# Performance work log

Hardware: AMD Instinct MI355X
Metric: run time of the kernel (lower is better)

## Reference

```python
import jax, jax.numpy as jnp
import numpy as np
import math

D_MODEL = 1024
N_HEADS = 16
SLOT_DIM = 64
N_SLOTS = 1024
TOP_K = 2
LN_EPS = 1e-5


def setup_inputs() -> dict:
    key = jax.random.key(0)
    ks = jax.random.split(key, 8)
    x = jax.random.normal(ks[0], (4, 2048, D_MODEL), dtype=jnp.float32)
    ln_gamma = jnp.ones((D_MODEL,), jnp.float32)
    ln_beta = jnp.zeros((D_MODEL,), jnp.float32)
    q_w = jax.random.normal(ks[1], (N_HEADS * SLOT_DIM, D_MODEL), jnp.float32) / math.sqrt(D_MODEL)
    q_b = jnp.zeros((N_HEADS * SLOT_DIM,), jnp.float32)
    slot_signatures = jax.random.normal(ks[2], (N_HEADS, N_SLOTS, SLOT_DIM), jnp.float32) * 0.5
    slot_values = jax.random.normal(ks[3], (N_HEADS, N_SLOTS, SLOT_DIM), jnp.float32) * 0.02
    out_w = jax.random.normal(ks[4], (D_MODEL, N_HEADS * SLOT_DIM), jnp.float32) / math.sqrt(N_HEADS * SLOT_DIM)
    out_b = jnp.zeros((D_MODEL,), jnp.float32)
    temperature = jnp.ones((1,), jnp.float32)
    return {"x": x, "ln_gamma": ln_gamma, "ln_beta": ln_beta, "q_w": q_w, "q_b": q_b,
            "slot_signatures": slot_signatures, "slot_values": slot_values,
            "out_w": out_w, "out_b": out_b, "temperature": temperature}


def _ternary_ste(sig):
    # forward = {-1,0,+1} quantization; backward = identity (straight-through)
    q = jnp.where(sig > 0.3, 1.0, jnp.where(sig < -0.3, -1.0, 0.0))
    return sig + jax.lax.stop_gradient(q - sig)


def reference(x, ln_gamma, ln_beta, q_w, q_b, slot_signatures, slot_values, out_w, out_b, temperature):
    B, T, D = x.shape
    # LayerNorm
    mean = jnp.mean(x, axis=-1, keepdims=True)
    var = jnp.var(x, axis=-1, keepdims=True)
    x_norm = (x - mean) * jax.lax.rsqrt(var + LN_EPS) * ln_gamma + ln_beta
    # Query projection -> [B, T, H, slot_dim]
    q = (x_norm @ q_w.T + q_b).reshape(B, T, N_HEADS, SLOT_DIM)
    sigs = _ternary_ste(slot_signatures)  # [H, S, d]
    scores = jnp.einsum('bthd,hsd->bths', q, sigs)
    scores = scores / (temperature * math.sqrt(SLOT_DIM))  # [B, T, H, S]
    # top-k routing
    topk_scores, slot_idx = jax.lax.top_k(scores, TOP_K)  # [B, T, H, K]
    weights = jax.nn.softmax(topk_scores, axis=-1)
    # gather selected slot values: [B, T, H, K, d]
    h_idx = jnp.arange(N_HEADS)[None, None, :, None]
    selected = slot_values[h_idx, slot_idx]
    read = jnp.sum(selected * weights[..., None], axis=3)  # [B, T, H, d]
    read = read.reshape(B, T, N_HEADS * SLOT_DIM)
    out = read @ out_w.T + out_b
    return x + out
```

## Files before the change

kernel.cpp:

```cpp
#include <hip/hip_runtime.h>

typedef unsigned short u16;
typedef unsigned int   u32;
typedef float f32x4 __attribute__((ext_vector_type(4)));
typedef __bf16 bf16x8 __attribute__((ext_vector_type(8)));

__device__ __forceinline__ u16 f2bf(float f){
  u32 u = __float_as_uint(f);
  u += 0x7fffu + ((u >> 16) & 1u);
  return (u16)(u >> 16);
}

__device__ __forceinline__ void gld16(const void* g, void* l){
  __builtin_amdgcn_global_load_lds((const __attribute__((address_space(1))) u32*)g,
                                   (__attribute__((address_space(3))) u32*)l, 16, 0, 0);
}

__global__ __launch_bounds__(256) void convert_kernel(
    const float* __restrict__ qw, const float* __restrict__ ow,
    const float* __restrict__ sg,
    u16* __restrict__ qwb, u16* __restrict__ owb, u16* __restrict__ sgb){
  int i = blockIdx.x * 256 + threadIdx.x;
  qwb[i] = f2bf(qw[i]);
  owb[i] = f2bf(ow[i]);
  float s = sg[i];
  float t = (s > 0.3f) ? 1.0f : ((s < -0.3f) ? -1.0f : 0.0f);
  sgb[i] = f2bf(t);
}

__global__ __launch_bounds__(256) void ln_kernel(
    const float* __restrict__ x, const float* __restrict__ g,
    const float* __restrict__ b, u16* __restrict__ xn){
  const int t = blockIdx.x, tid = threadIdx.x;
  f32x4 v = *(const f32x4*)(x + (size_t)t * 1024 + tid * 4);
  float s  = v[0] + v[1] + v[2] + v[3];
  float ss = v[0]*v[0] + v[1]*v[1] + v[2]*v[2] + v[3]*v[3];
  for (int off = 32; off; off >>= 1){
    s  += __shfl_down(s, off);
    ss += __shfl_down(ss, off);
  }
  __shared__ float red[8];
  int w = tid >> 6;
  if ((tid & 63) == 0){ red[w] = s; red[4 + w] = ss; }
  __syncthreads();
  s  = red[0] + red[1] + red[2] + red[3];
  ss = red[4] + red[5] + red[6] + red[7];
  float mean = s * (1.0f / 1024.0f);
  float var  = ss * (1.0f / 1024.0f) - mean * mean;
  float rs   = rsqrtf(var + 1e-5f);
  f32x4 gv = *(const f32x4*)(g + tid * 4);
  f32x4 bv = *(const f32x4*)(b + tid * 4);
  float y0 = (v[0]-mean)*rs*gv[0]+bv[0];
  float y1 = (v[1]-mean)*rs*gv[1]+bv[1];
  float y2 = (v[2]-mean)*rs*gv[2]+bv[2];
  float y3 = (v[3]-mean)*rs*gv[3]+bv[3];
  uint2 pk;
  pk.x = (u32)f2bf(y0) | ((u32)f2bf(y1) << 16);
  pk.y = (u32)f2bf(y2) | ((u32)f2bf(y3) << 16);
  *(uint2*)(xn + (size_t)t * 1024 + tid * 4) = pk;
}

__global__ __launch_bounds__(256, 2) void gemm_bt(
    const u16* __restrict__ A, const u16* __restrict__ B,
    const float* __restrict__ bias, const float* __restrict__ resid,
    float* __restrict__ outf, u16* __restrict__ outb, int mode){
  __shared__ u16 As[128 * 64];
  __shared__ u16 Bs[128 * 64];
  const int tid = threadIdx.x;
  const int m0 = blockIdx.y * 128, n0 = blockIdx.x * 128;
  const int w = tid >> 6, lane = tid & 63, lm = lane & 15, quad = lane >> 4;
  const int wm = (w & 1) * 64, wn = (w >> 1) * 64;
  const int lr = lane >> 3;
  const int lg = (lane & 7) ^ lr;
  const f32x4 fz = {0.f, 0.f, 0.f, 0.f};
  f32x4 acc[4][4];
  #pragma unroll
  for (int i = 0; i < 4; ++i)
    #pragma unroll
    for (int j = 0; j < 4; ++j) acc[i][j] = fz;

  const u16* gA = A + (size_t)(m0 + w * 32 + lr) * 1024 + lg * 8;
  const u16* gB = B + (size_t)(n0 + w * 32 + lr) * 1024 + lg * 8;
  u16* lA = &As[(w * 32) * 64];
  u16* lB = &Bs[(w * 32) * 64];
  const int sw = lm & 7;

  for (int kt = 0; kt < 16; ++kt){
    #pragma unroll
    for (int sub = 0; sub < 4; ++sub){
      gld16(gA + (size_t)(sub * 8) * 1024 + kt * 64, lA + sub * 8 * 64);
      gld16(gB + (size_t)(sub * 8) * 1024 + kt * 64, lB + sub * 8 * 64);
    }
    __syncthreads();
    #pragma unroll
    for (int kk = 0; kk < 2; ++kk){
      const int ch = ((quad + kk * 4) ^ sw) * 8;
      bf16x8 afr[4], bfr[4];
      #pragma unroll
      for (int i = 0; i < 4; ++i)
        afr[i] = *(const bf16x8*)(&As[(wm + i * 16 + lm) * 64 + ch]);
      #pragma unroll
      for (int j = 0; j < 4; ++j)
        bfr[j] = *(const bf16x8*)(&Bs[(wn + j * 16 + lm) * 64 + ch]);
      #pragma unroll
      for (int i = 0; i < 4; ++i)
        #pragma unroll
        for (int j = 0; j < 4; ++j)
          acc[i][j] = __builtin_amdgcn_mfma_f32_16x16x32_bf16(afr[i], bfr[j], acc[i][j], 0, 0, 0);
    }
    __syncthreads();
  }

  #pragma unroll
  for (int i = 0; i < 4; ++i){
    #pragma unroll
    for (int r = 0; r < 4; ++r){
      int grow = m0 + wm + i * 16 + quad * 4 + r;
      #pragma unroll
      for (int j = 0; j < 4; ++j){
        int gcol = n0 + wn + j * 16 + lm;
        float v = acc[i][j][r] + bias[gcol];
        if (mode){
          v += resid[(size_t)grow * 1024 + gcol];
          outf[(size_t)grow * 1024 + gcol] = v;
        } else {
          outb[(size_t)grow * 1024 + gcol] = f2bf(v);
        }
      }
    }
  }
}

__global__ __launch_bounds__(256) void route_kernel(
    const u16* __restrict__ q, const u16* __restrict__ sig,
    const float* __restrict__ V, const float* __restrict__ temp,
    u16* __restrict__ rd){
  const int h = blockIdx.y;
  const int t0 = blockIdx.x * 64;
  const int tid = threadIdx.x, w = tid >> 6, lane = tid & 63;
  const int lm = lane & 15, quad = lane >> 4;

  __shared__ u16 sbuf[2][64 * 64];
  __shared__ float fw1[64], fw2[64];
  __shared__ int   fi1[64], fi2[64];

  const u16* qrow = q + (size_t)(t0 + w * 16 + lm) * 1024 + h * 64;
  bf16x8 a0 = *(const bf16x8*)(qrow + quad * 8);
  bf16x8 a1 = *(const bf16x8*)(qrow + 32 + quad * 8);

  const u16* sigh = sig + (size_t)h * 65536;

  auto stage = [&](int t, int b){
    #pragma unroll
    for (int r = 0; r < 2; ++r){
      int c = tid + r * 256;
      int s = c >> 3, gl = c & 7;
      int g = gl ^ (s & 7);
      uint4 v = *(const uint4*)(sigh + (size_t)t * 4096 + s * 64 + g * 8);
      *(uint4*)(&sbuf[b][c * 8]) = v;
    }
  };

  float v1[4], v2[4]; int j1[4], j2[4];
  #pragma unroll
  for (int r = 0; r < 4; ++r){ v1[r] = -3e38f; v2[r] = -3e38f; j1[r] = 0; j2[r] = 0; }

  const int swz = lm & 7;
  stage(0, 0);
  for (int t = 0; t < 16; ++t){
    __syncthreads();
    if (t + 1 < 16) stage(t + 1, (t + 1) & 1);
    const u16* buf = sbuf[t & 1];
    #pragma unroll
    for (int ss = 0; ss < 4; ++ss){
      int srow = ss * 16 + lm;
      int c0 = (quad ^ swz) * 8;
      bf16x8 b0 = *(const bf16x8*)(&buf[srow * 64 + c0]);
      bf16x8 b1 = *(const bf16x8*)(&buf[srow * 64 + (c0 ^ 32)]);
      f32x4 acc = {0.f, 0.f, 0.f, 0.f};
      acc = __builtin_amdgcn_mfma_f32_16x16x32_bf16(a0, b0, acc, 0, 0, 0);
      acc = __builtin_amdgcn_mfma_f32_16x16x32_bf16(a1, b1, acc, 0, 0, 0);
      int sidx = t * 64 + srow;
      #pragma unroll
      for (int r = 0; r < 4; ++r){
        float v = acc[r];
        bool g1 = v > v1[r];
        bool g2 = v > v2[r];
        float nv2 = g1 ? v1[r] : (g2 ? v : v2[r]);
        int   nj2 = g1 ? j1[r] : (g2 ? sidx : j2[r]);
        v2[r] = nv2; j2[r] = nj2;
        v1[r] = g1 ? v : v1[r];
        j1[r] = g1 ? sidx : j1[r];
      }
    }
  }
  #pragma unroll
  for (int off = 1; off < 16; off <<= 1){
    #pragma unroll
    for (int r = 0; r < 4; ++r){
      float ov1 = __shfl_xor(v1[r], off);
      int   oj1 = __shfl_xor(j1[r], off);
      float ov2 = __shfl_xor(v2[r], off);
      int   oj2 = __shfl_xor(j2[r], off);
      bool gt = ov1 > v1[r];
      float ca = gt ? v1[r] : ov1; int cja = gt ? j1[r] : oj1;
      float cb = gt ? ov2  : v2[r]; int cjb = gt ? oj2  : j2[r];
      v1[r] = gt ? ov1 : v1[r];  j1[r] = gt ? oj1 : j1[r];
      bool gb = cb > ca;
      v2[r] = gb ? cb : ca;  j2[r] = gb ? cjb : cja;
    }
  }
  if (lm == 0){
    float tsc = 1.0f / (temp[0] * 8.0f);
    #pragma unroll
    for (int r = 0; r < 4; ++r){
      int tok = w * 16 + quad * 4 + r;
      float ex = expf((v2[r] - v1[r]) * tsc);
      float iw = 1.0f / (1.0f + ex);
      fw1[tok] = iw; fw2[tok] = ex * iw;
      fi1[tok] = j1[r]; fi2[tok] = j2[r];
    }
  }
  __syncthreads();
  int tok = tid >> 2, d0 = (tid & 3) * 16;
  const float* va = V + ((size_t)h * 1024 + fi1[tok]) * 64 + d0;
  const float* vb = V + ((size_t)h * 1024 + fi2[tok]) * 64 + d0;
  float W1 = fw1[tok], W2 = fw2[tok];
  u32 pk[8];
  #pragma unroll
  for (int d = 0; d < 16; d += 4){
    f32x4 x1 = *(const f32x4*)(va + d);
    f32x4 x2 = *(const f32x4*)(vb + d);
    #pragma unroll
    for (int e = 0; e < 4; e += 2){
      float y0 = W1 * x1[e]     + W2 * x2[e];
      float y1 = W1 * x1[e + 1] + W2 * x2[e + 1];
      pk[(d + e) >> 1] = (u32)f2bf(y0) | ((u32)f2bf(y1) << 16);
    }
  }
  u16* dst = rd + (size_t)(t0 + tok) * 1024 + h * 64 + d0;
  uint4 o0 = {pk[0], pk[1], pk[2], pk[3]};
  uint4 o1 = {pk[4], pk[5], pk[6], pk[7]};
  *(uint4*)dst = o0;
  *(uint4*)(dst + 8) = o1;
}

extern "C" void kernel_launch(void* const* d_in, const int* in_sizes, int n_in,
                              void* d_out, int out_size, void* d_ws, size_t ws_size,
                              hipStream_t stream){
  const float* x    = (const float*)d_in[0];
  const float* lng  = (const float*)d_in[1];
  const float* lnb  = (const float*)d_in[2];
  const float* qw   = (const float*)d_in[3];
  const float* qb   = (const float*)d_in[4];
  const float* sig  = (const float*)d_in[5];
  const float* sv   = (const float*)d_in[6];
  const float* ow   = (const float*)d_in[7];
  const float* ob   = (const float*)d_in[8];
  const float* temp = (const float*)d_in[9];
  float* out = (float*)d_out;

  char* ws = (char*)d_ws;
  u16* xn   = (u16*)(ws);
  u16* qwb  = (u16*)(ws + 16777216);
  u16* owb  = (u16*)(ws + 16777216 + 2097152);
  u16* sgb  = (u16*)(ws + 16777216 + 2 * 2097152);
  u16* qb16 = (u16*)(ws + 16777216 + 3 * 2097152);
  u16* rdb  = xn;

  convert_kernel<<<4096, 256, 0, stream>>>(qw, ow, sig, qwb, owb, sgb);
  ln_kernel<<<8192, 256, 0, stream>>>(x, lng, lnb, xn);
  gemm_bt<<<dim3(8, 64), 256, 0, stream>>>(xn, qwb, qb, nullptr, nullptr, qb16, 0);
  route_kernel<<<dim3(128, 16), 256, 0, stream>>>(qb16, sgb, sv, temp, rdb);
  gemm_bt<<<dim3(8, 64), 256, 0, stream>>>(rdb, owb, ob, x, out, nullptr, 1);
}
```

Before: 224.5 us.

## Rework routing kernel with 32x32 MFMA, packed-index top-2 and async LDS staging

The routing kernel now handles 128 tokens per block and computes scores with 32x32x16 bf16 MFMAs instead of 16x16x32. It packs the slot index into the low 10 mantissa bits of each score, so the top-2 update becomes fmax plus fmed3 with no index registers or branches, and the cross-lane reduction shrinks to match. Signature tiles are staged with global_load_lds directly into a swizzled LDS layout. The packed keys drop low mantissa bits, which can change routing when scores nearly tie, and the larger tile halves the grid and raises register use.

Result: faster. 217.0 us (-3.4%).

```diff
diff --git a/kernel.cpp b/kernel.cpp
--- a/kernel.cpp
+++ b/kernel.cpp
@@ -2,7 +2,8 @@
 
 typedef unsigned short u16;
 typedef unsigned int   u32;
-typedef float f32x4 __attribute__((ext_vector_type(4)));
+typedef float f32x4  __attribute__((ext_vector_type(4)));
+typedef float f32x16 __attribute__((ext_vector_type(16)));
 typedef __bf16 bf16x8 __attribute__((ext_vector_type(8)));
 
 __device__ __forceinline__ u16 f2bf(float f){
@@ -136,113 +137,117 @@
     const float* __restrict__ V, const float* __restrict__ temp,
     u16* __restrict__ rd){
   const int h = blockIdx.y;
-  const int t0 = blockIdx.x * 64;
+  const int t0 = blockIdx.x * 128;
   const int tid = threadIdx.x, w = tid >> 6, lane = tid & 63;
-  const int lm = lane & 15, quad = lane >> 4;
-
-  __shared__ u16 sbuf[2][64 * 64];
-  __shared__ float fw1[64], fw2[64];
-  __shared__ int   fi1[64], fi2[64];
-
-  const u16* qrow = q + (size_t)(t0 + w * 16 + lm) * 1024 + h * 64;
-  bf16x8 a0 = *(const bf16x8*)(qrow + quad * 8);
-  bf16x8 a1 = *(const bf16x8*)(qrow + 32 + quad * 8);
+  const int col = lane & 31, half = lane >> 5;
+
+  __shared__ u16 sbuf[2][128 * 64];
+  __shared__ float fw1[128], fw2[128];
+  __shared__ int   fi1[128], fi2[128];
+
+  const u16* qrow = q + (size_t)(t0 + w * 32 + col) * 1024 + h * 64 + half * 8;
+  bf16x8 afr[4];
+  #pragma unroll
+  for (int c = 0; c < 4; ++c) afr[c] = *(const bf16x8*)(qrow + c * 16);
 
   const u16* sigh = sig + (size_t)h * 65536;
 
+  const int lr = lane >> 3, lg = (lane & 7) ^ lr;
+  const u16* ssrc = sigh + (size_t)(w * 32 + lr) * 64 + lg * 8;
   auto stage = [&](int t, int b){
-    #pragma unroll
-    for (int r = 0; r < 2; ++r){
-      int c = tid + r * 256;
-      int s = c >> 3, gl = c & 7;
-      int g = gl ^ (s & 7);
-      uint4 v = *(const uint4*)(sigh + (size_t)t * 4096 + s * 64 + g * 8);
-      *(uint4*)(&sbuf[b][c * 8]) = v;
-    }
+    const u16* s0 = ssrc + (size_t)t * 128 * 64;
+    u16* d0 = &sbuf[b][(w * 32) * 64];
+    #pragma unroll
+    for (int sub = 0; sub < 4; ++sub)
+      gld16(s0 + sub * 8 * 64, d0 + sub * 8 * 64);
   };
 
-  float v1[4], v2[4]; int j1[4], j2[4];
-  #pragma unroll
-  for (int r = 0; r < 4; ++r){ v1[r] = -3e38f; v2[r] = -3e38f; j1[r] = 0; j2[r] = 0; }
-
-  const int swz = lm & 7;
+  int p0 = ((0 + half) ^ (col & 7)) * 8;
+  int p1 = ((2 + half) ^ (col & 7)) * 8;
+  int p2 = ((4 + half) ^ (col & 7)) * 8;
+  int p3 = ((6 + half) ^ (col & 7)) * 8;
+
+  float v1[16], v2[16];
+  #pragma unroll
+  for (int r = 0; r < 16; ++r){ v1[r] = -3.0e38f; v2[r] = -3.0e38f; }
+
   stage(0, 0);
-  for (int t = 0; t < 16; ++t){
+  for (int t = 0; t < 8; ++t){
     __syncthreads();
-    if (t + 1 < 16) stage(t + 1, (t + 1) & 1);
+    if (t < 7) stage(t + 1, (t + 1) & 1);
     const u16* buf = sbuf[t & 1];
     #pragma unroll
-    for (int ss = 0; ss < 4; ++ss){
-      int srow = ss * 16 + lm;
-      int c0 = (quad ^ swz) * 8;
-      bf16x8 b0 = *(const bf16x8*)(&buf[srow * 64 + c0]);
-      bf16x8 b1 = *(const bf16x8*)(&buf[srow * 64 + (c0 ^ 32)]);
-      f32x4 acc = {0.f, 0.f, 0.f, 0.f};
-      acc = __builtin_amdgcn_mfma_f32_16x16x32_bf16(a0, b0, acc, 0, 0, 0);
-      acc = __builtin_amdgcn_mfma_f32_16x16x32_bf16(a1, b1, acc, 0, 0, 0);
-      int sidx = t * 64 + srow;
-      #pragma unroll
-      for (int r = 0; r < 4; ++r){
-        float v = acc[r];
-        bool g1 = v > v1[r];
-        bool g2 = v > v2[r];
-        float nv2 = g1 ? v1[r] : (g2 ? v : v2[r]);
-        int   nj2 = g1 ? j1[r] : (g2 ? sidx : j2[r]);
-        v2[r] = nv2; j2[r] = nj2;
-        v1[r] = g1 ? v : v1[r];
-        j1[r] = g1 ? sidx : j1[r];
+    for (int sbl = 0; sbl < 4; ++sbl){
+      const u16* srow = &buf[(sbl * 32 + col) * 64];
+      bf16x8 b0 = *(const bf16x8*)(srow + p0);
+      bf16x8 b1 = *(const bf16x8*)(srow + p1);
+      bf16x8 b2 = *(const bf16x8*)(srow + p2);
+      bf16x8 b3 = *(const bf16x8*)(srow + p3);
+      f32x16 acc = {};
+      acc = __builtin_amdgcn_mfma_f32_32x32x16_bf16(afr[0], b0, acc, 0, 0, 0);
+      acc = __builtin_amdgcn_mfma_f32_32x32x16_bf16(afr[1], b1, acc, 0, 0, 0);
+      acc = __builtin_amdgcn_mfma_f32_32x32x16_bf16(afr[2], b2, acc, 0, 0, 0);
+      acc = __builtin_amdgcn_mfma_f32_32x32x16_bf16(afr[3], b3, acc, 0, 0, 0);
+      u32 sidx = (u32)(t * 128 + sbl * 32 + col);
+      #pragma unroll
+      for (int r = 0; r < 16; ++r){
+        u32 u = __float_as_uint(acc[r]);
+        float key = __uint_as_float((u & 0xFFFFFC00u) | sidx);
+        float o1 = v1[r];
+        v1[r] = fmaxf(o1, key);
+        v2[r] = __builtin_amdgcn_fmed3f(o1, v2[r], key);
       }
     }
   }
-  #pragma unroll
-  for (int off = 1; off < 16; off <<= 1){
-    #pragma unroll
-    for (int r = 0; r < 4; ++r){
-      float ov1 = __shfl_xor(v1[r], off);
-      int   oj1 = __shfl_xor(j1[r], off);
-      float ov2 = __shfl_xor(v2[r], off);
-      int   oj2 = __shfl_xor(j2[r], off);
-      bool gt = ov1 > v1[r];
-      float ca = gt ? v1[r] : ov1; int cja = gt ? j1[r] : oj1;
-      float cb = gt ? ov2  : v2[r]; int cjb = gt ? oj2  : j2[r];
-      v1[r] = gt ? ov1 : v1[r];  j1[r] = gt ? oj1 : j1[r];
-      bool gb = cb > ca;
-      v2[r] = gb ? cb : ca;  j2[r] = gb ? cjb : cja;
-    }
-  }
-  if (lm == 0){
+
+  #pragma unroll
+  for (int off = 1; off < 32; off <<= 1){
+    #pragma unroll
+    for (int r = 0; r < 16; ++r){
+      float b1v = __shfl_xor(v1[r], off);
+      float b2v = __shfl_xor(v2[r], off);
+      float a1 = v1[r];
+      v1[r] = fmaxf(a1, b1v);
+      v2[r] = __builtin_amdgcn_fmed3f(a1, b1v, fmaxf(v2[r], b2v));
+    }
+  }
+
+  if (col == 0){
     float tsc = 1.0f / (temp[0] * 8.0f);
     #pragma unroll
-    for (int r = 0; r < 4; ++r){
-      int tok = w * 16 + quad * 4 + r;
-      float ex = expf((v2[r] - v1[r]) * tsc);
+    for (int r = 0; r < 16; ++r){
+      int row = (r & 3) + 8 * (r >> 2) + 4 * half;
+      int tl = w * 32 + row;
+      u32 u1 = __float_as_uint(v1[r]);
+      u32 u2 = __float_as_uint(v2[r]);
+      float s1 = __uint_as_float(u1 & 0xFFFFFC00u);
+      float s2 = __uint_as_float(u2 & 0xFFFFFC00u);
+      float ex = __expf((s2 - s1) * tsc);
       float iw = 1.0f / (1.0f + ex);
-      fw1[tok] = iw; fw2[tok] = ex * iw;
-      fi1[tok] = j1[r]; fi2[tok] = j2[r];
+      fw1[tl] = iw; fw2[tl] = ex * iw;
+      fi1[tl] = (int)(u1 & 1023u); fi2[tl] = (int)(u2 & 1023u);
     }
   }
   __syncthreads();
-  int tok = tid >> 2, d0 = (tid & 3) * 16;
-  const float* va = V + ((size_t)h * 1024 + fi1[tok]) * 64 + d0;
-  const float* vb = V + ((size_t)h * 1024 + fi2[tok]) * 64 + d0;
-  float W1 = fw1[tok], W2 = fw2[tok];
-  u32 pk[8];
-  #pragma unroll
-  for (int d = 0; d < 16; d += 4){
-    f32x4 x1 = *(const f32x4*)(va + d);
-    f32x4 x2 = *(const f32x4*)(vb + d);
-    #pragma unroll
-    for (int e = 0; e < 4; e += 2){
-      float y0 = W1 * x1[e]     + W2 * x2[e];
-      float y1 = W1 * x1[e + 1] + W2 * x2[e + 1];
-      pk[(d + e) >> 1] = (u32)f2bf(y0) | ((u32)f2bf(y1) << 16);
-    }
-  }
-  u16* dst = rd + (size_t)(t0 + tok) * 1024 + h * 64 + d0;
-  uint4 o0 = {pk[0], pk[1], pk[2], pk[3]};
-  uint4 o1 = {pk[4], pk[5], pk[6], pk[7]};
-  *(uint4*)dst = o0;
-  *(uint4*)(dst + 8) = o1;
+
+  int tl = tid >> 1, d0 = (tid & 1) * 32;
+  const float* va = V + ((size_t)h * 1024 + fi1[tl]) * 64 + d0;
+  const float* vb = V + ((size_t)h * 1024 + fi2[tl]) * 64 + d0;
+  float W1 = fw1[tl], W2 = fw2[tl];
+  u16* dst = rd + (size_t)(t0 + tl) * 1024 + h * 64 + d0;
+  #pragma unroll
+  for (int g = 0; g < 4; ++g){
+    f32x4 xa = *(const f32x4*)(va + g * 8);
+    f32x4 xb = *(const f32x4*)(va + g * 8 + 4);
+    f32x4 ya = *(const f32x4*)(vb + g * 8);
+    f32x4 yb = *(const f32x4*)(vb + g * 8 + 4);
+    uint4 o;
+    o.x = (u32)f2bf(W1*xa[0]+W2*ya[0]) | ((u32)f2bf(W1*xa[1]+W2*ya[1]) << 16);
+    o.y = (u32)f2bf(W1*xa[2]+W2*ya[2]) | ((u32)f2bf(W1*xa[3]+W2*ya[3]) << 16);
+    o.z = (u32)f2bf(W1*xb[0]+W2*yb[0]) | ((u32)f2bf(W1*xb[1]+W2*yb[1]) << 16);
+    o.w = (u32)f2bf(W1*xb[2]+W2*yb[2]) | ((u32)f2bf(W1*xb[3]+W2*yb[3]) << 16);
+    *(uint4*)(dst + g * 8) = o;
+  }
 }
 
 extern "C" void kernel_launch(void* const* d_in, const int* in_sizes, int n_in,
@@ -271,6 +276,6 @@
   convert_kernel<<<4096, 256, 0, stream>>>(qw, ow, sig, qwb, owb, sgb);
   ln_kernel<<<8192, 256, 0, stream>>>(x, lng, lnb, xn);
   gemm_bt<<<dim3(8, 64), 256, 0, stream>>>(xn, qwb, qb, nullptr, nullptr, qb16, 0);
-  route_kernel<<<dim3(128, 16), 256, 0, stream>>>(qb16, sgb, sv, temp, rdb);
+  route_kernel<<<dim3(64, 16), 256, 0, stream>>>(qb16, sgb, sv, temp, rdb);
   gemm_bt<<<dim3(8, 64), 256, 0, stream>>>(rdb, owb, ob, x, out, nullptr, 1);
 }
```
